# Kernel tuning notes

Measured on AMD Instinct MI355X. Metric: run time of the kernel, lower is better.

Reference implementation:

```python
import jax, jax.numpy as jnp
import numpy as np

B, TQ, TK = 8, 2048, 4096
DIM_IMG, DIM_TXT, HS = 512, 128, 64


def _make_freqs(seqlen, half_dim):
    # standard RoPE angles: theta = pos * 10000^(-2i/d); stored as [T, half_dim, 2] = (cos, sin)
    inv = 1.0 / (10000.0 ** (np.arange(0, half_dim, dtype=np.float32) / half_dim))
    ang = np.arange(seqlen, dtype=np.float32)[:, None] * inv[None, :]
    return jnp.asarray(np.stack([np.cos(ang), np.sin(ang)], axis=-1))


def _rot_complex(x, f):
    # x: [B, T, D]; f: [T, D//2, 2] (real, imag). Complex multiply on (even, odd) pairs.
    xr = x.reshape(*x.shape[:-1], -1, 2)
    a, b = xr[..., 0], xr[..., 1]
    fr, fi = f[None, ..., 0], f[None, ..., 1]
    out = jnp.stack([a * fr - b * fi, a * fi + b * fr], axis=-1)
    return out.reshape(x.shape)


def _rot2d(x, fx, fy):
    vx, vy = jnp.split(x, 2, axis=-1)
    return jnp.concatenate([_rot_complex(vx, fx), _rot_complex(vy, fy)], axis=-1)


def setup_inputs() -> dict:
    key = jax.random.key(0)
    k1, k2, k3, k4, k5 = jax.random.split(key, 5)
    return {
        "x_image": jax.random.normal(k1, (B, TK, DIM_IMG), dtype=jnp.float32),
        "x_text_emb": jax.random.normal(k2, (B, TQ, DIM_TXT), dtype=jnp.float32),
        "x_latex_mask": jax.random.randint(k3, (B, TQ), 0, 2, dtype=jnp.int32),
        "freqs_latex": _make_freqs(TQ, HS // 2),
        "freqs_img_x": _make_freqs(TK, HS // 4),
        "freqs_img_y": _make_freqs(TK, HS // 4),
        "Wk": jax.random.normal(k4, (HS, DIM_IMG), dtype=jnp.float32) * (DIM_IMG ** -0.5),
        "Wq": jax.random.normal(k5, (HS, DIM_TXT), dtype=jnp.float32) * (DIM_TXT ** -0.5),
        "Wv": jax.random.normal(jax.random.fold_in(key, 7), (HS, DIM_IMG), dtype=jnp.float32) * (DIM_IMG ** -0.5),
    }


def reference(x_image, x_text_emb, x_latex_mask, freqs_latex, freqs_img_x, freqs_img_y, Wk, Wq, Wv):
    C = x_image.shape[-1]  # original divides by sqrt of image embed dim (512), not head_size
    k = jnp.einsum("btc,hc->bth", x_image, Wk)
    k = jax.lax.stop_gradient(_rot2d(k, freqs_img_x, freqs_img_y))  # torch.no_grad in source
    q = jnp.einsum("bsc,hc->bsh", x_text_emb, Wq)
    q = jax.lax.stop_gradient(_rot_complex(q, freqs_latex))  # torch.no_grad in source
    v = jnp.einsum("btc,hc->bth", x_image, Wv)
    wei = jnp.einsum("bsh,bth->bst", q, k) / (C ** 0.5)  # [B, TQ, TK]
    softwei = jax.nn.softmax(wei, axis=-1)
    out = jnp.einsum("bst,bth->bsh", softwei, v)
    return out
```

## Files before the change

### kernel.cpp

```cpp
#include <hip/hip_runtime.h>


#define B_    8
#define TQ_   2048
#define TK_   4096
#define DIMG  512
#define DTXT  128
#define HS_   64
#define NSPL  4
#define TSPL  (TK_ / NSPL)

typedef float f32x4 __attribute__((ext_vector_type(4)));
typedef __bf16 bf16x8 __attribute__((ext_vector_type(8)));

static __device__ __forceinline__ unsigned short f2bf(float x) {
    unsigned u = __float_as_uint(x);
    u += 0x7fffu + ((u >> 16) & 1u);
    return (unsigned short)(u >> 16);
}

__global__ __launch_bounds__(256) void proj_kv_kernel(
    const float* __restrict__ x_image, const float* __restrict__ fx,
    const float* __restrict__ fy, const float* __restrict__ Wk,
    const float* __restrict__ Wv, unsigned short* __restrict__ K_ws,
    unsigned short* __restrict__ Vt_ws)
{
    __shared__ unsigned short Xc[64][72];
    __shared__ unsigned short Wc[128][72];

    const int tid = threadIdx.x;
    const int b  = blockIdx.x & 7;
    const int t0 = (blockIdx.x >> 3) * 64;
    const int w  = tid >> 6;
    const int l  = tid & 63;
    const int col  = l & 15;
    const int hi4  = l >> 4;

    f32x4 acc[8];
    #pragma unroll
    for (int g = 0; g < 8; ++g) acc[g] = (f32x4){0.f, 0.f, 0.f, 0.f};

    for (int kc = 0; kc < DIMG; kc += 64) {
        #pragma unroll
        for (int m = 0; m < 4; ++m) {
            int lin = tid + 256 * m;
            int r = lin >> 4;
            int c = (lin & 15) * 4;
            float4 v = *(const float4*)(x_image + ((size_t)(b * TK_ + t0 + r)) * DIMG + kc + c);
            unsigned lo = (unsigned)f2bf(v.x) | ((unsigned)f2bf(v.y) << 16);
            unsigned hi = (unsigned)f2bf(v.z) | ((unsigned)f2bf(v.w) << 16);
            *(uint2*)&Xc[r][c] = make_uint2(lo, hi);
        }
        #pragma unroll
        for (int m = 0; m < 8; ++m) {
            int lin = tid + 256 * m;
            int r = lin >> 4;
            int c = (lin & 15) * 4;
            const float* src = (r < 64) ? (Wk + (size_t)r * DIMG + kc + c)
                                        : (Wv + (size_t)(r - 64) * DIMG + kc + c);
            float4 v = *(const float4*)src;
            unsigned lo = (unsigned)f2bf(v.x) | ((unsigned)f2bf(v.y) << 16);
            unsigned hi = (unsigned)f2bf(v.z) | ((unsigned)f2bf(v.w) << 16);
            *(uint2*)&Wc[r][c] = make_uint2(lo, hi);
        }
        __syncthreads();

        bf16x8 a0 = *(const bf16x8*)&Xc[16 * w + col][hi4 * 8];
        bf16x8 a1 = *(const bf16x8*)&Xc[16 * w + col][hi4 * 8 + 32];
        #pragma unroll
        for (int g = 0; g < 8; ++g) {
            bf16x8 b0 = *(const bf16x8*)&Wc[g * 16 + col][hi4 * 8];
            bf16x8 b1 = *(const bf16x8*)&Wc[g * 16 + col][hi4 * 8 + 32];
            acc[g] = __builtin_amdgcn_mfma_f32_16x16x32_bf16(a0, b0, acc[g], 0, 0, 0);
            acc[g] = __builtin_amdgcn_mfma_f32_16x16x32_bf16(a1, b1, acc[g], 0, 0, 0);
        }
        __syncthreads();
    }

    const int rbase = hi4 * 4;
    #pragma unroll
    for (int g = 0; g < 4; ++g) {
        int h = g * 16 + col;
        const float* ftab = (h < 32) ? fx : fy;
        int i = (h & 31) >> 1;
        float sgn = (h & 1) ? 1.f : -1.f;
        #pragma unroll
        for (int j = 0; j < 4; ++j) {
            int t = t0 + 16 * w + rbase + j;
            float v = acc[g][j];
            float p = __shfl_xor(v, 1);
            float2 cs = *(const float2*)(ftab + ((size_t)t * 16 + i) * 2);
            float o = v * cs.x + sgn * p * cs.y;
            K_ws[((size_t)(b * TK_ + t)) * HS_ + h] = f2bf(o);
        }
    }
    #pragma unroll
    for (int g = 4; g < 8; ++g) {
        int h = (g - 4) * 16 + col;
        int tb = t0 + 16 * w + rbase;
        unsigned lo = (unsigned)f2bf(acc[g][0]) | ((unsigned)f2bf(acc[g][1]) << 16);
        unsigned hi = (unsigned)f2bf(acc[g][2]) | ((unsigned)f2bf(acc[g][3]) << 16);
        *(uint2*)&Vt_ws[((size_t)(b * HS_ + h)) * TK_ + tb] = make_uint2(lo, hi);
    }
}

__global__ __launch_bounds__(256) void proj_q_kernel(
    const float* __restrict__ x_text, const float* __restrict__ fl,
    const float* __restrict__ Wq, unsigned short* __restrict__ Q_ws)
{
    __shared__ unsigned short Xc[64][72];
    __shared__ unsigned short Wc[64][72];

    const int tid = threadIdx.x;
    const int b  = blockIdx.x & 7;
    const int s0 = (blockIdx.x >> 3) * 64;
    const int w  = tid >> 6;
    const int l  = tid & 63;
    const int col = l & 15;
    const int hi4 = l >> 4;

    f32x4 acc[4];
    #pragma unroll
    for (int g = 0; g < 4; ++g) acc[g] = (f32x4){0.f, 0.f, 0.f, 0.f};

    for (int kc = 0; kc < DTXT; kc += 64) {
        #pragma unroll
        for (int m = 0; m < 4; ++m) {
            int lin = tid + 256 * m;
            int r = lin >> 4;
            int c = (lin & 15) * 4;
            float4 v = *(const float4*)(x_text + ((size_t)(b * TQ_ + s0 + r)) * DTXT + kc + c);
            unsigned lo = (unsigned)f2bf(v.x) | ((unsigned)f2bf(v.y) << 16);
            unsigned hi = (unsigned)f2bf(v.z) | ((unsigned)f2bf(v.w) << 16);
            *(uint2*)&Xc[r][c] = make_uint2(lo, hi);
        }
        #pragma unroll
        for (int m = 0; m < 4; ++m) {
            int lin = tid + 256 * m;
            int r = lin >> 4;
            int c = (lin & 15) * 4;
            float4 v = *(const float4*)(Wq + (size_t)r * DTXT + kc + c);
            unsigned lo = (unsigned)f2bf(v.x) | ((unsigned)f2bf(v.y) << 16);
            unsigned hi = (unsigned)f2bf(v.z) | ((unsigned)f2bf(v.w) << 16);
            *(uint2*)&Wc[r][c] = make_uint2(lo, hi);
        }
        __syncthreads();

        bf16x8 a0 = *(const bf16x8*)&Xc[16 * w + col][hi4 * 8];
        bf16x8 a1 = *(const bf16x8*)&Xc[16 * w + col][hi4 * 8 + 32];
        #pragma unroll
        for (int g = 0; g < 4; ++g) {
            bf16x8 b0 = *(const bf16x8*)&Wc[g * 16 + col][hi4 * 8];
            bf16x8 b1 = *(const bf16x8*)&Wc[g * 16 + col][hi4 * 8 + 32];
            acc[g] = __builtin_amdgcn_mfma_f32_16x16x32_bf16(a0, b0, acc[g], 0, 0, 0);
            acc[g] = __builtin_amdgcn_mfma_f32_16x16x32_bf16(a1, b1, acc[g], 0, 0, 0);
        }
        __syncthreads();
    }

    const float SCALE = 0.044194173824159216f;
    const int rbase = hi4 * 4;
    #pragma unroll
    for (int g = 0; g < 4; ++g) {
        int h = g * 16 + col;
        int i = h >> 1;
        float sgn = (h & 1) ? 1.f : -1.f;
        #pragma unroll
        for (int j = 0; j < 4; ++j) {
            int s = s0 + 16 * w + rbase + j;
            float v = acc[g][j];
            float p = __shfl_xor(v, 1);
            float2 cs = *(const float2*)(fl + ((size_t)s * 32 + i) * 2);
            float o = (v * cs.x + sgn * p * cs.y) * SCALE;
            Q_ws[((size_t)(b * TQ_ + s)) * HS_ + h] = f2bf(o);
        }
    }
}

__global__ __launch_bounds__(512, 4) void attn_partial_kernel(
    const unsigned short* __restrict__ Q_ws,
    const unsigned short* __restrict__ K_ws,
    const unsigned short* __restrict__ Vt_ws,
    float* __restrict__ num_ws, float* __restrict__ den_ws)
{
    __shared__ unsigned short Kt[128][72];
    __shared__ unsigned short Vv[64][136];
    __shared__ unsigned short Pl[8][16][136];

    const int tid  = threadIdx.x;
    const int bid  = blockIdx.x;
    const int b    = bid & 7;
    const int rest = bid >> 3;
    const int stile = rest & 15;
    const int split = rest >> 4;
    const int s0 = stile * 128;
    const int w  = tid >> 6;
    const int l  = tid & 63;
    const int col = l & 15;
    const int hi4 = l >> 4;

    const int srow = s0 + 16 * w + col;
    bf16x8 q0 = *(const bf16x8*)(Q_ws + ((size_t)(b * TQ_ + srow)) * HS_ + hi4 * 8);
    bf16x8 q1 = *(const bf16x8*)(Q_ws + ((size_t)(b * TQ_ + srow)) * HS_ + hi4 * 8 + 32);

    f32x4 oacc[4];
    #pragma unroll
    for (int g = 0; g < 4; ++g) oacc[g] = (f32x4){0.f, 0.f, 0.f, 0.f};
    f32x4 den = (f32x4){0.f, 0.f, 0.f, 0.f};

    const int tbase = split * TSPL;
    for (int ti = 0; ti < TSPL / 128; ++ti) {
        const int tt = tbase + ti * 128;
        #pragma unroll
        for (int m = 0; m < 2; ++m) {
            int lin = tid + 512 * m;
            int r = lin >> 3;
            int h = (lin & 7) * 8;
            *(uint4*)&Kt[r][h] =
                *(const uint4*)(K_ws + ((size_t)(b * TK_ + tt + r)) * HS_ + h);
        }
        #pragma unroll
        for (int m = 0; m < 2; ++m) {
            int lin = tid + 512 * m;
            int h  = lin >> 4;
            int tk = (lin & 15) * 8;
            *(uint4*)&Vv[h][tk] =
                *(const uint4*)(Vt_ws + ((size_t)(b * HS_ + h)) * TK_ + tt + tk);
        }
        __syncthreads();

        #pragma unroll
        for (int n = 0; n < 8; ++n) {
            bf16x8 k0 = *(const bf16x8*)&Kt[n * 16 + col][hi4 * 8];
            bf16x8 k1 = *(const bf16x8*)&Kt[n * 16 + col][hi4 * 8 + 32];
            f32x4 p = (f32x4){0.f, 0.f, 0.f, 0.f};
            p = __builtin_amdgcn_mfma_f32_16x16x32_bf16(q0, k0, p, 0, 0, 0);
            p = __builtin_amdgcn_mfma_f32_16x16x32_bf16(q1, k1, p, 0, 0, 0);
            #pragma unroll
            for (int j = 0; j < 4; ++j) {
                float e = __expf(p[j]);
                unsigned short eb = f2bf(e);
                den[j] += __uint_as_float((unsigned)eb << 16);
                Pl[w][hi4 * 4 + j][n * 16 + col] = eb;
            }
        }
        asm volatile("s_waitcnt lgkmcnt(0)" ::: "memory");
        __builtin_amdgcn_sched_barrier(0);

        #pragma unroll
        for (int c = 0; c < 4; ++c) {
            bf16x8 pa = *(const bf16x8*)&Pl[w][col][c * 32 + hi4 * 8];
            #pragma unroll
            for (int g = 0; g < 4; ++g) {
                bf16x8 vb = *(const bf16x8*)&Vv[g * 16 + col][c * 32 + hi4 * 8];
                oacc[g] = __builtin_amdgcn_mfma_f32_16x16x32_bf16(pa, vb, oacc[g], 0, 0, 0);
            }
        }
        __syncthreads();
    }

    #pragma unroll
    for (int m = 1; m < 16; m <<= 1) {
        #pragma unroll
        for (int j = 0; j < 4; ++j) den[j] += __shfl_xor(den[j], m);
    }

    const size_t sec = (size_t)(split * B_ + b) * TQ_;
    #pragma unroll
    for (int g = 0; g < 4; ++g) {
        #pragma unroll
        for (int j = 0; j < 4; ++j) {
            int s = s0 + 16 * w + hi4 * 4 + j;
            num_ws[(sec + s) * HS_ + g * 16 + col] = oacc[g][j];
        }
    }
    if (col == 0) {
        #pragma unroll
        for (int j = 0; j < 4; ++j) {
            int s = s0 + 16 * w + hi4 * 4 + j;
            den_ws[sec + s] = den[j];
        }
    }
}

__global__ __launch_bounds__(256) void attn_reduce_kernel(
    const float* __restrict__ num_ws, const float* __restrict__ den_ws,
    float* __restrict__ out)
{
    const int idx = blockIdx.x * 256 + threadIdx.x;
    const int row = idx >> 4;
    const size_t spl4 = (size_t)B_ * TQ_ * HS_ / 4;
    const float4* n4 = (const float4*)num_ws;
    float4 a = n4[idx];
    float4 v1 = n4[idx + spl4];
    float4 v2 = n4[idx + 2 * spl4];
    float4 v3 = n4[idx + 3 * spl4];
    a.x += v1.x + v2.x + v3.x;
    a.y += v1.y + v2.y + v3.y;
    a.z += v1.z + v2.z + v3.z;
    a.w += v1.w + v2.w + v3.w;
    float d = den_ws[row] + den_ws[row + B_ * TQ_] +
              den_ws[row + 2 * B_ * TQ_] + den_ws[row + 3 * B_ * TQ_];
    float inv = 1.f / d;
    a.x *= inv; a.y *= inv; a.z *= inv; a.w *= inv;
    ((float4*)out)[idx] = a;
}

__global__ __launch_bounds__(256) void attn_kernel(
    const unsigned short* __restrict__ Q_ws,
    const unsigned short* __restrict__ K_ws,
    const unsigned short* __restrict__ Vt_ws,
    float* __restrict__ out)
{
    __shared__ unsigned short Kt[128][72];
    __shared__ unsigned short Vv[64][136];
    __shared__ unsigned short Pl[4][16][136];

    const int tid = threadIdx.x;
    const int b  = blockIdx.x & 7;
    const int s0 = (blockIdx.x >> 3) * 64;
    const int w  = tid >> 6;
    const int l  = tid & 63;
    const int col = l & 15;
    const int hi4 = l >> 4;

    const int srow = s0 + 16 * w + col;
    bf16x8 q0 = *(const bf16x8*)(Q_ws + ((size_t)(b * TQ_ + srow)) * HS_ + hi4 * 8);
    bf16x8 q1 = *(const bf16x8*)(Q_ws + ((size_t)(b * TQ_ + srow)) * HS_ + hi4 * 8 + 32);

    f32x4 oacc[4];
    #pragma unroll
    for (int g = 0; g < 4; ++g) oacc[g] = (f32x4){0.f, 0.f, 0.f, 0.f};
    f32x4 den = (f32x4){0.f, 0.f, 0.f, 0.f};

    for (int tt = 0; tt < TK_; tt += 128) {
        #pragma unroll
        for (int m = 0; m < 4; ++m) {
            int lin = tid + 256 * m;
            int r = lin >> 3;
            int h = (lin & 7) * 8;
            *(uint4*)&Kt[r][h] =
                *(const uint4*)(K_ws + ((size_t)(b * TK_ + tt + r)) * HS_ + h);
        }
        #pragma unroll
        for (int m = 0; m < 4; ++m) {
            int lin = tid + 256 * m;
            int h  = lin >> 4;
            int tk = (lin & 15) * 8;
            *(uint4*)&Vv[h][tk] =
                *(const uint4*)(Vt_ws + ((size_t)(b * HS_ + h)) * TK_ + tt + tk);
        }
        __syncthreads();

        #pragma unroll
        for (int n = 0; n < 8; ++n) {
            bf16x8 k0 = *(const bf16x8*)&Kt[n * 16 + col][hi4 * 8];
            bf16x8 k1 = *(const bf16x8*)&Kt[n * 16 + col][hi4 * 8 + 32];
            f32x4 p = (f32x4){0.f, 0.f, 0.f, 0.f};
            p = __builtin_amdgcn_mfma_f32_16x16x32_bf16(q0, k0, p, 0, 0, 0);
            p = __builtin_amdgcn_mfma_f32_16x16x32_bf16(q1, k1, p, 0, 0, 0);
            #pragma unroll
            for (int j = 0; j < 4; ++j) {
                float e = __expf(p[j]);
                unsigned short eb = f2bf(e);
                den[j] += __uint_as_float((unsigned)eb << 16);
                Pl[w][hi4 * 4 + j][n * 16 + col] = eb;
            }
        }
        asm volatile("s_waitcnt lgkmcnt(0)" ::: "memory");
        __builtin_amdgcn_sched_barrier(0);

        #pragma unroll
        for (int c = 0; c < 4; ++c) {
            bf16x8 pa = *(const bf16x8*)&Pl[w][col][c * 32 + hi4 * 8];
            #pragma unroll
            for (int g = 0; g < 4; ++g) {
                bf16x8 vb = *(const bf16x8*)&Vv[g * 16 + col][c * 32 + hi4 * 8];
                oacc[g] = __builtin_amdgcn_mfma_f32_16x16x32_bf16(pa, vb, oacc[g], 0, 0, 0);
            }
        }
        __syncthreads();
    }

    #pragma unroll
    for (int m = 1; m < 16; m <<= 1) {
        #pragma unroll
        for (int j = 0; j < 4; ++j) den[j] += __shfl_xor(den[j], m);
    }
    float inv[4];
    #pragma unroll
    for (int j = 0; j < 4; ++j) inv[j] = 1.f / den[j];

    #pragma unroll
    for (int g = 0; g < 4; ++g) {
        #pragma unroll
        for (int j = 0; j < 4; ++j) {
            int s = s0 + 16 * w + hi4 * 4 + j;
            out[((size_t)(b * TQ_ + s)) * HS_ + g * 16 + col] = oacc[g][j] * inv[j];
        }
    }
}

extern "C" void kernel_launch(void* const* d_in, const int* in_sizes, int n_in,
                              void* d_out, int out_size, void* d_ws, size_t ws_size,
                              hipStream_t stream) {
    const float* x_image = (const float*)d_in[0];
    const float* x_text  = (const float*)d_in[1];
    const float* fl      = (const float*)d_in[3];
    const float* fx      = (const float*)d_in[4];
    const float* fy      = (const float*)d_in[5];
    const float* Wk      = (const float*)d_in[6];
    const float* Wq      = (const float*)d_in[7];
    const float* Wv      = (const float*)d_in[8];

    unsigned short* K_ws  = (unsigned short*)d_ws;
    unsigned short* Vt_ws = K_ws + (size_t)B_ * TK_ * HS_;
    unsigned short* Q_ws  = Vt_ws + (size_t)B_ * TK_ * HS_;
    float* out = (float*)d_out;

    const size_t kvq_bytes = (size_t)(2 * B_ * TK_ * HS_ + B_ * TQ_ * HS_) * 2;
    const size_t num_bytes = (size_t)NSPL * B_ * TQ_ * HS_ * 4;
    const size_t den_bytes = (size_t)NSPL * B_ * TQ_ * 4;

    proj_kv_kernel<<<dim3(512), dim3(256), 0, stream>>>(x_image, fx, fy, Wk, Wv, K_ws, Vt_ws);
    proj_q_kernel<<<dim3(256), dim3(256), 0, stream>>>(x_text, fl, Wq, Q_ws);

    if (ws_size >= kvq_bytes + num_bytes + den_bytes) {
        float* num_ws = (float*)((char*)d_ws + kvq_bytes);
        float* den_ws = num_ws + (size_t)NSPL * B_ * TQ_ * HS_;
        attn_partial_kernel<<<dim3(512), dim3(512), 0, stream>>>(Q_ws, K_ws, Vt_ws, num_ws, den_ws);
        attn_reduce_kernel<<<dim3(B_ * TQ_ * HS_ / 4 / 256), dim3(256), 0, stream>>>(num_ws, den_ws, out);
    } else {
        attn_kernel<<<dim3(256), dim3(256), 0, stream>>>(Q_ws, K_ws, Vt_ws, out);
    }
}
```

Before: 175.4 us.

## Fuse Q and KV projections into one launch and double-buffer tile loads

Merges the KV and Q projection kernels into a single 768-block launch, with blocks branching on their index, so one kernel launch and the tail gap between launches go away. The KV projection gets double-buffered LDS staging so global loads of the next K-chunk overlap MFMA work on the current one. The Q branch loads the full 128-wide reduction in one pass. The attention partial kernel prefetches the next K/V tile into registers during compute and stores it to LDS after a barrier. The larger LDS footprint (about 54 KB) and extra live registers may reduce occupancy.

```diff
diff --git a/kernel.cpp b/kernel.cpp
--- a/kernel.cpp
+++ b/kernel.cpp
@@ -19,160 +19,169 @@
     return (unsigned short)(u >> 16);
 }
 
-__global__ __launch_bounds__(256) void proj_kv_kernel(
+#define STAGE_KV(XBUF, WBUF, kc)                                                      \
+    {                                                                                 \
+        _Pragma("unroll")                                                             \
+        for (int m = 0; m < 4; ++m) {                                                 \
+            int lin = tid + 256 * m;                                                  \
+            int r = lin >> 4;                                                         \
+            int c = (lin & 15) * 4;                                                   \
+            float4 v = *(const float4*)(x_image + ((size_t)(b * TK_ + t0 + r)) * DIMG + (kc) + c); \
+            unsigned lo = (unsigned)f2bf(v.x) | ((unsigned)f2bf(v.y) << 16);          \
+            unsigned hi = (unsigned)f2bf(v.z) | ((unsigned)f2bf(v.w) << 16);          \
+            *(uint2*)&XBUF[r][c] = make_uint2(lo, hi);                                \
+        }                                                                             \
+        _Pragma("unroll")                                                             \
+        for (int m = 0; m < 8; ++m) {                                                 \
+            int lin = tid + 256 * m;                                                  \
+            int r = lin >> 4;                                                         \
+            int c = (lin & 15) * 4;                                                   \
+            const float* src = (r < 64) ? (Wk + (size_t)r * DIMG + (kc) + c)          \
+                                        : (Wv + (size_t)(r - 64) * DIMG + (kc) + c);  \
+            float4 v = *(const float4*)src;                                           \
+            unsigned lo = (unsigned)f2bf(v.x) | ((unsigned)f2bf(v.y) << 16);          \
+            unsigned hi = (unsigned)f2bf(v.z) | ((unsigned)f2bf(v.w) << 16);          \
+            *(uint2*)&WBUF[r][c] = make_uint2(lo, hi);                                \
+        }                                                                             \
+    }
+
+#define COMPUTE_KV(XBUF, WBUF)                                                        \
+    {                                                                                 \
+        bf16x8 a0 = *(const bf16x8*)&XBUF[16 * w + col][hi4 * 8];                     \
+        bf16x8 a1 = *(const bf16x8*)&XBUF[16 * w + col][hi4 * 8 + 32];                \
+        _Pragma("unroll")                                                             \
+        for (int g = 0; g < 8; ++g) {                                                 \
+            bf16x8 b0 = *(const bf16x8*)&WBUF[g * 16 + col][hi4 * 8];                 \
+            bf16x8 b1 = *(const bf16x8*)&WBUF[g * 16 + col][hi4 * 8 + 32];            \
+            acc[g] = __builtin_amdgcn_mfma_f32_16x16x32_bf16(a0, b0, acc[g], 0, 0, 0);\
+            acc[g] = __builtin_amdgcn_mfma_f32_16x16x32_bf16(a1, b1, acc[g], 0, 0, 0);\
+        }                                                                             \
+    }
+
+__global__ __launch_bounds__(256) void proj_fused_kernel(
     const float* __restrict__ x_image, const float* __restrict__ fx,
     const float* __restrict__ fy, const float* __restrict__ Wk,
-    const float* __restrict__ Wv, unsigned short* __restrict__ K_ws,
-    unsigned short* __restrict__ Vt_ws)
+    const float* __restrict__ Wv, const float* __restrict__ x_text,
+    const float* __restrict__ fl, const float* __restrict__ Wq,
+    unsigned short* __restrict__ K_ws, unsigned short* __restrict__ Vt_ws,
+    unsigned short* __restrict__ Q_ws)
 {
-    __shared__ unsigned short Xc[64][72];
-    __shared__ unsigned short Wc[128][72];
+    __shared__ __align__(16) unsigned short lds[27648];
 
     const int tid = threadIdx.x;
-    const int b  = blockIdx.x & 7;
-    const int t0 = (blockIdx.x >> 3) * 64;
-    const int w  = tid >> 6;
-    const int l  = tid & 63;
-    const int col  = l & 15;
-    const int hi4  = l >> 4;
-
-    f32x4 acc[8];
-    #pragma unroll
-    for (int g = 0; g < 8; ++g) acc[g] = (f32x4){0.f, 0.f, 0.f, 0.f};
-
-    for (int kc = 0; kc < DIMG; kc += 64) {
-        #pragma unroll
-        for (int m = 0; m < 4; ++m) {
-            int lin = tid + 256 * m;
-            int r = lin >> 4;
-            int c = (lin & 15) * 4;
-            float4 v = *(const float4*)(x_image + ((size_t)(b * TK_ + t0 + r)) * DIMG + kc + c);
-            unsigned lo = (unsigned)f2bf(v.x) | ((unsigned)f2bf(v.y) << 16);
-            unsigned hi = (unsigned)f2bf(v.z) | ((unsigned)f2bf(v.w) << 16);
-            *(uint2*)&Xc[r][c] = make_uint2(lo, hi);
-        }
-        #pragma unroll
-        for (int m = 0; m < 8; ++m) {
-            int lin = tid + 256 * m;
-            int r = lin >> 4;
-            int c = (lin & 15) * 4;
-            const float* src = (r < 64) ? (Wk + (size_t)r * DIMG + kc + c)
-                                        : (Wv + (size_t)(r - 64) * DIMG + kc + c);
-            float4 v = *(const float4*)src;
-            unsigned lo = (unsigned)f2bf(v.x) | ((unsigned)f2bf(v.y) << 16);
-            unsigned hi = (unsigned)f2bf(v.z) | ((unsigned)f2bf(v.w) << 16);
-            *(uint2*)&Wc[r][c] = make_uint2(lo, hi);
-        }
-        __syncthreads();
-
-        bf16x8 a0 = *(const bf16x8*)&Xc[16 * w + col][hi4 * 8];
-        bf16x8 a1 = *(const bf16x8*)&Xc[16 * w + col][hi4 * 8 + 32];
-        #pragma unroll
-        for (int g = 0; g < 8; ++g) {
-            bf16x8 b0 = *(const bf16x8*)&Wc[g * 16 + col][hi4 * 8];
-            bf16x8 b1 = *(const bf16x8*)&Wc[g * 16 + col][hi4 * 8 + 32];
-            acc[g] = __builtin_amdgcn_mfma_f32_16x16x32_bf16(a0, b0, acc[g], 0, 0, 0);
-            acc[g] = __builtin_amdgcn_mfma_f32_16x16x32_bf16(a1, b1, acc[g], 0, 0, 0);
-        }
-        __syncthreads();
-    }
-
-    const int rbase = hi4 * 4;
-    #pragma unroll
-    for (int g = 0; g < 4; ++g) {
-        int h = g * 16 + col;
-        const float* ftab = (h < 32) ? fx : fy;
-        int i = (h & 31) >> 1;
-        float sgn = (h & 1) ? 1.f : -1.f;
-        #pragma unroll
-        for (int j = 0; j < 4; ++j) {
-            int t = t0 + 16 * w + rbase + j;
-            float v = acc[g][j];
-            float p = __shfl_xor(v, 1);
-            float2 cs = *(const float2*)(ftab + ((size_t)t * 16 + i) * 2);
-            float o = v * cs.x + sgn * p * cs.y;
-            K_ws[((size_t)(b * TK_ + t)) * HS_ + h] = f2bf(o);
-        }
-    }
-    #pragma unroll
-    for (int g = 4; g < 8; ++g) {
-        int h = (g - 4) * 16 + col;
-        int tb = t0 + 16 * w + rbase;
-        unsigned lo = (unsigned)f2bf(acc[g][0]) | ((unsigned)f2bf(acc[g][1]) << 16);
-        unsigned hi = (unsigned)f2bf(acc[g][2]) | ((unsigned)f2bf(acc[g][3]) << 16);
-        *(uint2*)&Vt_ws[((size_t)(b * HS_ + h)) * TK_ + tb] = make_uint2(lo, hi);
-    }
-}
-
-__global__ __launch_bounds__(256) void proj_q_kernel(
-    const float* __restrict__ x_text, const float* __restrict__ fl,
-    const float* __restrict__ Wq, unsigned short* __restrict__ Q_ws)
-{
-    __shared__ unsigned short Xc[64][72];
-    __shared__ unsigned short Wc[64][72];
-
-    const int tid = threadIdx.x;
-    const int b  = blockIdx.x & 7;
-    const int s0 = (blockIdx.x >> 3) * 64;
+    const int bid = blockIdx.x;
     const int w  = tid >> 6;
     const int l  = tid & 63;
     const int col = l & 15;
     const int hi4 = l >> 4;
 
-    f32x4 acc[4];
-    #pragma unroll
-    for (int g = 0; g < 4; ++g) acc[g] = (f32x4){0.f, 0.f, 0.f, 0.f};
-
-    for (int kc = 0; kc < DTXT; kc += 64) {
-        #pragma unroll
-        for (int m = 0; m < 4; ++m) {
+    if (bid < 512) {
+        auto Xc0 = (unsigned short(*)[72])(lds);
+        auto Xc1 = (unsigned short(*)[72])(lds + 4608);
+        auto Wc0 = (unsigned short(*)[72])(lds + 9216);
+        auto Wc1 = (unsigned short(*)[72])(lds + 18432);
+
+        const int b  = bid & 7;
+        const int t0 = (bid >> 3) * 64;
+
+        f32x4 acc[8];
+        #pragma unroll
+        for (int g = 0; g < 8; ++g) acc[g] = (f32x4){0.f, 0.f, 0.f, 0.f};
+
+        STAGE_KV(Xc0, Wc0, 0);
+        __syncthreads();
+        for (int c2 = 0; c2 < 8; c2 += 2) {
+            STAGE_KV(Xc1, Wc1, (c2 + 1) * 64);
+            COMPUTE_KV(Xc0, Wc0);
+            __syncthreads();
+            if (c2 + 2 < 8) STAGE_KV(Xc0, Wc0, (c2 + 2) * 64);
+            COMPUTE_KV(Xc1, Wc1);
+            __syncthreads();
+        }
+
+        const int rbase = hi4 * 4;
+        #pragma unroll
+        for (int g = 0; g < 4; ++g) {
+            int h = g * 16 + col;
+            const float* ftab = (h < 32) ? fx : fy;
+            int i = (h & 31) >> 1;
+            float sgn = (h & 1) ? 1.f : -1.f;
+            #pragma unroll
+            for (int j = 0; j < 4; ++j) {
+                int t = t0 + 16 * w + rbase + j;
+                float v = acc[g][j];
+                float p = __shfl_xor(v, 1);
+                float2 cs = *(const float2*)(ftab + ((size_t)t * 16 + i) * 2);
+                float o = v * cs.x + sgn * p * cs.y;
+                K_ws[((size_t)(b * TK_ + t)) * HS_ + h] = f2bf(o);
+            }
+        }
+        #pragma unroll
+        for (int g = 4; g < 8; ++g) {
+            int h = (g - 4) * 16 + col;
+            int tb = t0 + 16 * w + rbase;
+            unsigned lo = (unsigned)f2bf(acc[g][0]) | ((unsigned)f2bf(acc[g][1]) << 16);
+            unsigned hi = (unsigned)f2bf(acc[g][2]) | ((unsigned)f2bf(acc[g][3]) << 16);
+            *(uint2*)&Vt_ws[((size_t)(b * HS_ + h)) * TK_ + tb] = make_uint2(lo, hi);
+        }
+    } else {
+        auto Xq = (unsigned short(*)[136])(lds);
+        auto Wl = (unsigned short(*)[136])(lds + 8704);
+
+        const int b  = bid & 7;
+        const int s0 = ((bid - 512) >> 3) * 64;
+
+        #pragma unroll
+        for (int m = 0; m < 8; ++m) {
             int lin = tid + 256 * m;
-            int r = lin >> 4;
-            int c = (lin & 15) * 4;
-            float4 v = *(const float4*)(x_text + ((size_t)(b * TQ_ + s0 + r)) * DTXT + kc + c);
+            int r = lin >> 5;
+            int c = (lin & 31) * 4;
+            float4 v = *(const float4*)(x_text + ((size_t)(b * TQ_ + s0 + r)) * DTXT + c);
             unsigned lo = (unsigned)f2bf(v.x) | ((unsigned)f2bf(v.y) << 16);
             unsigned hi = (unsigned)f2bf(v.z) | ((unsigned)f2bf(v.w) << 16);
-            *(uint2*)&Xc[r][c] = make_uint2(lo, hi);
-        }
-        #pragma unroll
-        for (int m = 0; m < 4; ++m) {
+            *(uint2*)&Xq[r][c] = make_uint2(lo, hi);
+        }
+        #pragma unroll
+        for (int m = 0; m < 8; ++m) {
             int lin = tid + 256 * m;
-            int r = lin >> 4;
-            int c = (lin & 15) * 4;
-            float4 v = *(const float4*)(Wq + (size_t)r * DTXT + kc + c);
+            int r = lin >> 5;
+            int c = (lin & 31) * 4;
+            float4 v = *(const float4*)(Wq + (size_t)r * DTXT + c);
             unsigned lo = (unsigned)f2bf(v.x) | ((unsigned)f2bf(v.y) << 16);
             unsigned hi = (unsigned)f2bf(v.z) | ((unsigned)f2bf(v.w) << 16);
-            *(uint2*)&Wc[r][c] = make_uint2(lo, hi);
-        }
-        __syncthreads();
-
-        bf16x8 a0 = *(const bf16x8*)&Xc[16 * w + col][hi4 * 8];
-        bf16x8 a1 = *(const bf16x8*)&Xc[16 * w + col][hi4 * 8 + 32];
+            *(uint2*)&Wl[r][c] = make_uint2(lo, hi);
+        }
+        __syncthreads();
+
+        f32x4 acc[4];
+        #pragma unroll
+        for (int g = 0; g < 4; ++g) acc[g] = (f32x4){0.f, 0.f, 0.f, 0.f};
+        #pragma unroll
+        for (int kk = 0; kk < 4; ++kk) {
+            bf16x8 a = *(const bf16x8*)&Xq[16 * w + col][hi4 * 8 + kk * 32];
+            #pragma unroll
+            for (int g = 0; g < 4; ++g) {
+                bf16x8 bb = *(const bf16x8*)&Wl[g * 16 + col][hi4 * 8 + kk * 32];
+                acc[g] = __builtin_amdgcn_mfma_f32_16x16x32_bf16(a, bb, acc[g], 0, 0, 0);
+            }
+        }
+
+        const float SCALE = 0.044194173824159216f;
+        const int rbase = hi4 * 4;
         #pragma unroll
         for (int g = 0; g < 4; ++g) {
-            bf16x8 b0 = *(const bf16x8*)&Wc[g * 16 + col][hi4 * 8];
-            bf16x8 b1 = *(const bf16x8*)&Wc[g * 16 + col][hi4 * 8 + 32];
-            acc[g] = __builtin_amdgcn_mfma_f32_16x16x32_bf16(a0, b0, acc[g], 0, 0, 0);
-            acc[g] = __builtin_amdgcn_mfma_f32_16x16x32_bf16(a1, b1, acc[g], 0, 0, 0);
-        }
-        __syncthreads();
-    }
-
-    const float SCALE = 0.044194173824159216f;
-    const int rbase = hi4 * 4;
-    #pragma unroll
-    for (int g = 0; g < 4; ++g) {
-        int h = g * 16 + col;
-        int i = h >> 1;
-        float sgn = (h & 1) ? 1.f : -1.f;
-        #pragma unroll
-        for (int j = 0; j < 4; ++j) {
-            int s = s0 + 16 * w + rbase + j;
-            float v = acc[g][j];
-            float p = __shfl_xor(v, 1);
-            float2 cs = *(const float2*)(fl + ((size_t)s * 32 + i) * 2);
-            float o = (v * cs.x + sgn * p * cs.y) * SCALE;
-            Q_ws[((size_t)(b * TQ_ + s)) * HS_ + h] = f2bf(o);
+            int h = g * 16 + col;
+            int i = h >> 1;
+            float sgn = (h & 1) ? 1.f : -1.f;
+            #pragma unroll
+            for (int j = 0; j < 4; ++j) {
+                int s = s0 + 16 * w + rbase + j;
+                float v = acc[g][j];
+                float p = __shfl_xor(v, 1);
+                float2 cs = *(const float2*)(fl + ((size_t)s * 32 + i) * 2);
+                float o = (v * cs.x + sgn * p * cs.y) * SCALE;
+                Q_ws[((size_t)(b * TQ_ + s)) * HS_ + h] = f2bf(o);
+            }
         }
     }
 }
@@ -209,25 +218,29 @@
     f32x4 den = (f32x4){0.f, 0.f, 0.f, 0.f};
 
     const int tbase = split * TSPL;
+    const int lin1 = tid + 512;
+    const int kr_r0 = tid >> 3,  kr_h0 = (tid & 7) * 8;
+    const int kr_r1 = lin1 >> 3, kr_h1 = (lin1 & 7) * 8;
+    const int vr_h0 = tid >> 4,  vr_t0 = (tid & 15) * 8;
+    const int vr_h1 = lin1 >> 4, vr_t1 = (lin1 & 15) * 8;
+
+    *(uint4*)&Kt[kr_r0][kr_h0] = *(const uint4*)(K_ws + ((size_t)(b * TK_ + tbase + kr_r0)) * HS_ + kr_h0);
+    *(uint4*)&Kt[kr_r1][kr_h1] = *(const uint4*)(K_ws + ((size_t)(b * TK_ + tbase + kr_r1)) * HS_ + kr_h1);
+    *(uint4*)&Vv[vr_h0][vr_t0] = *(const uint4*)(Vt_ws + ((size_t)(b * HS_ + vr_h0)) * TK_ + tbase + vr_t0);
+    *(uint4*)&Vv[vr_h1][vr_t1] = *(const uint4*)(Vt_ws + ((size_t)(b * HS_ + vr_h1)) * TK_ + tbase + vr_t1);
+    __syncthreads();
+
     for (int ti = 0; ti < TSPL / 128; ++ti) {
         const int tt = tbase + ti * 128;
-        #pragma unroll
-        for (int m = 0; m < 2; ++m) {
-            int lin = tid + 512 * m;
-            int r = lin >> 3;
-            int h = (lin & 7) * 8;
-            *(uint4*)&Kt[r][h] =
-                *(const uint4*)(K_ws + ((size_t)(b * TK_ + tt + r)) * HS_ + h);
-        }
-        #pragma unroll
-        for (int m = 0; m < 2; ++m) {
-            int lin = tid + 512 * m;
-            int h  = lin >> 4;
-            int tk = (lin & 15) * 8;
-            *(uint4*)&Vv[h][tk] =
-                *(const uint4*)(Vt_ws + ((size_t)(b * HS_ + h)) * TK_ + tt + tk);
-        }
-        __syncthreads();
+        const bool pre = (ti + 1 < TSPL / 128);
+        uint4 kr0, kr1, vr0, vr1;
+        if (pre) {
+            const int tn = tt + 128;
+            kr0 = *(const uint4*)(K_ws + ((size_t)(b * TK_ + tn + kr_r0)) * HS_ + kr_h0);
+            kr1 = *(const uint4*)(K_ws + ((size_t)(b * TK_ + tn + kr_r1)) * HS_ + kr_h1);
+            vr0 = *(const uint4*)(Vt_ws + ((size_t)(b * HS_ + vr_h0)) * TK_ + tn + vr_t0);
+            vr1 = *(const uint4*)(Vt_ws + ((size_t)(b * HS_ + vr_h1)) * TK_ + tn + vr_t1);
+        }
 
         #pragma unroll
         for (int n = 0; n < 8; ++n) {
@@ -255,6 +268,13 @@
                 bf16x8 vb = *(const bf16x8*)&Vv[g * 16 + col][c * 32 + hi4 * 8];
                 oacc[g] = __builtin_amdgcn_mfma_f32_16x16x32_bf16(pa, vb, oacc[g], 0, 0, 0);
             }
+        }
+        __syncthreads();
+        if (pre) {
+            *(uint4*)&Kt[kr_r0][kr_h0] = kr0;
+            *(uint4*)&Kt[kr_r1][kr_h1] = kr1;
+            *(uint4*)&Vv[vr_h0][vr_t0] = vr0;
+            *(uint4*)&Vv[vr_h1][vr_t1] = vr1;
         }
         __syncthreads();
     }
@@ -339,16 +359,14 @@
             int lin = tid + 256 * m;
             int r = lin >> 3;
             int h = (lin & 7) * 8;
-            *(uint4*)&Kt[r][h] =
-                *(const uint4*)(K_ws + ((size_t)(b * TK_ + tt + r)) * HS_ + h);
+            *(uint4*)&Kt[r][h] = *(const uint4*)(K_ws + ((size_t)(b * TK_ + tt + r)) * HS_ + h);
         }
         #pragma unroll
         for (int m = 0; m < 4; ++m) {
             int lin = tid + 256 * m;
             int h  = lin >> 4;
             int tk = (lin & 15) * 8;
-            *(uint4*)&Vv[h][tk] =
-                *(const uint4*)(Vt_ws + ((size_t)(b * HS_ + h)) * TK_ + tt + tk);
+            *(uint4*)&Vv[h][tk] = *(const uint4*)(Vt_ws + ((size_t)(b * HS_ + h)) * TK_ + tt + tk);
         }
         __syncthreads();
 
@@ -422,8 +440,8 @@
     const size_t num_bytes = (size_t)NSPL * B_ * TQ_ * HS_ * 4;
     const size_t den_bytes = (size_t)NSPL * B_ * TQ_ * 4;
 
-    proj_kv_kernel<<<dim3(512), dim3(256), 0, stream>>>(x_image, fx, fy, Wk, Wv, K_ws, Vt_ws);
-    proj_q_kernel<<<dim3(256), dim3(256), 0, stream>>>(x_text, fl, Wq, Q_ws);
+    proj_fused_kernel<<<dim3(768), dim3(256), 0, stream>>>(
+        x_image, fx, fy, Wk, Wv, x_text, fl, Wq, K_ws, Vt_ws, Q_ws);
 
     if (ws_size >= kvq_bytes + num_bytes + den_bytes) {
         float* num_ws = (float*)((char*)d_ws + kvq_bytes);
```

After: 161.5 us. -7.9%, faster.
